# Kernel optimization log

Hardware: AMD Instinct MI355X
Metric: run time of the kernel (lower is better)

The kernel has to match this reference:

```python
import jax, jax.numpy as jnp
import numpy as np
import math

# SH band constants (match torch source)
A0C0 = math.pi * (1.0 / math.sqrt(4.0 * math.pi))
A1C1 = (2.0 * math.pi / math.sqrt(3.0)) * (math.sqrt(3.0) / math.sqrt(4.0 * math.pi))
A2C2 = (2.0 * math.pi / math.sqrt(8.0)) * (3.0 * math.sqrt(5.0) / math.sqrt(12.0 * math.pi))
AMBIENT = 0.8
SIGMA = 1e-4   # BlendParams defaults
GAMMA = 1e-4
BG = (1.0, 1.0, 1.0)
ZNEAR, ZFAR = 1.0, 100.0
EPS = 1e-10

V, F = 100000, 200000
N, H, W, K = 2, 512, 512, 8


def setup_inputs() -> dict:
    key = jax.random.key(0)
    ks = jax.random.split(key, 8)
    verts_normals = jax.random.normal(ks[0], (V, 3), dtype=jnp.float32)
    verts_colors = jax.random.uniform(ks[1], (V, 3), dtype=jnp.float32)
    sh_coeffs = jax.random.normal(ks[2], (1, 9, 3), dtype=jnp.float32) * 0.3
    bary = jax.random.uniform(ks[3], (N, H, W, K, 3), dtype=jnp.float32) + 1e-3
    bary_coords = bary / jnp.sum(bary, axis=-1, keepdims=True)  # convex weights
    zbuf = ZNEAR + (ZFAR - ZNEAR) * jax.random.uniform(ks[4], (N, H, W, K), dtype=jnp.float32)
    dists = jax.random.normal(ks[5], (N, H, W, K), dtype=jnp.float32) * 1e-4  # signed pixel-to-edge dists
    faces = jax.random.randint(ks[6], (F, 3), 0, V, dtype=jnp.int64 if jax.config.jax_enable_x64 else jnp.int32)
    pix_to_face = jax.random.randint(ks[7], (N, H, W, K), -20000, F,
                                     dtype=jnp.int64 if jax.config.jax_enable_x64 else jnp.int32)
    return {"verts_normals": verts_normals, "verts_colors": verts_colors,
            "sh_coeffs": sh_coeffs, "bary_coords": bary_coords,
            "zbuf": zbuf, "dists": dists, "faces": faces, "pix_to_face": pix_to_face}


def _forward(verts_normals, verts_colors, sh_coeffs, bary_coords, zbuf, dists,
             faces, pix_to_face):
    # --- per-vertex SH shading ---
    sh = sh_coeffs.at[..., 0, :].add(AMBIENT)          # (1,9,3), ambient term
    nrm = jnp.maximum(jnp.linalg.norm(verts_normals, axis=-1, keepdims=True), 1e-6)
    n = verts_normals / nrm                            # (V,3)
    nx, ny, nz = n[..., 0], n[..., 1], n[..., 2]
    Y = jnp.stack([
        jnp.full(nx.shape, A0C0, dtype=n.dtype),
        -A1C1 * ny,
        A1C1 * nz,
        -A1C1 * nx,
        A2C2 * nx * ny,
        -A2C2 * ny * nz,
        A2C2 * 0.5 / math.sqrt(3.0) * (3.0 * nz * nz - 1.0),
        -A2C2 * nx * nz,
        A2C2 * 0.5 * (nx * nx - ny * ny),
    ], axis=-1)                                        # (V,9)
    shading = jnp.einsum('vn,nc->vc', Y, sh[0])        # (V,3)
    verts_colors_shaded = verts_colors * shading       # (V,3)

    # --- face gather + barycentric interpolation ---
    face_colors = verts_colors_shaded[faces]           # (F,3,3)
    mask = pix_to_face >= 0                            # (N,H,W,K)
    idx = jnp.where(mask, pix_to_face, 0)
    pix_face_vals = face_colors[idx]                   # (N,H,W,K,3,3)
    colors = jnp.sum(bary_coords[..., None] * pix_face_vals, axis=-2)  # (N,H,W,K,3)
    colors = jnp.where(mask[..., None], colors, 0.0)

    # --- softmax RGB blend ---
    maskf = mask.astype(colors.dtype)
    prob = jax.nn.sigmoid(-dists / SIGMA) * maskf                       # (N,H,W,K)
    alpha = jnp.prod(1.0 - prob, axis=-1)                               # (N,H,W)
    z_inv = (ZFAR - zbuf) / (ZFAR - ZNEAR) * maskf
    z_inv_max = jnp.maximum(jnp.max(z_inv, axis=-1, keepdims=True), EPS)
    weights_num = prob * jnp.exp((z_inv - z_inv_max) / GAMMA)
    delta = jnp.exp((EPS - z_inv_max) / GAMMA)                          # background weight
    denom = jnp.sum(weights_num, axis=-1, keepdims=True) + delta
    weighted_colors = jnp.sum(weights_num[..., None] * colors, axis=-2)  # (N,H,W,3)
    bg = jnp.asarray(BG, dtype=colors.dtype)
    rgb = (weighted_colors + delta * bg) / denom
    return jnp.concatenate([rgb, (1.0 - alpha)[..., None]], axis=-1)    # (N,H,W,4)


def reference(verts_normals, verts_colors, sh_coeffs, bary_coords, zbuf, dists,
              faces, pix_to_face):
    return _forward(verts_normals, verts_colors, sh_coeffs, bary_coords, zbuf,
                    dists, faces, pix_to_face)
```

## Files before the change

### kernel.cpp

```cpp
#include <hip/hip_runtime.h>
#include <math.h>

namespace {

constexpr float kA0C0    = 0.8862269254527580f;
constexpr float kA1C1    = 1.7724538509055159f;
constexpr float kA2C2    = 2.4270324670f;
constexpr float kAmbient = 0.8f;
constexpr float kSigma   = 1e-4f;
constexpr float kGamma   = 1e-4f;
constexpr float kEps     = 1e-10f;
constexpr float kZnear   = 1.0f;
constexpr float kZfar    = 100.0f;
constexpr int   kK       = 8;

__global__ void shade_verts_kernel(const float* __restrict__ vn,
                                   const float* __restrict__ vc,
                                   const float* __restrict__ sh,
                                   float* __restrict__ vs, int V) {
  int v = blockIdx.x * blockDim.x + threadIdx.x;
  if (v >= V) return;
  float nx = vn[3 * v + 0], ny = vn[3 * v + 1], nz = vn[3 * v + 2];
  float nrm = fmaxf(sqrtf(nx * nx + ny * ny + nz * nz), 1e-6f);
  nx /= nrm; ny /= nrm; nz /= nrm;
  float Y[9];
  Y[0] = kA0C0;
  Y[1] = -kA1C1 * ny;
  Y[2] =  kA1C1 * nz;
  Y[3] = -kA1C1 * nx;
  Y[4] =  kA2C2 * nx * ny;
  Y[5] = -kA2C2 * ny * nz;
  Y[6] =  kA2C2 * (0.5f / 1.7320508075688772f) * (3.0f * nz * nz - 1.0f);
  Y[7] = -kA2C2 * nx * nz;
  Y[8] =  kA2C2 * 0.5f * (nx * nx - ny * ny);
#pragma unroll
  for (int c = 0; c < 3; ++c) {
    float s = Y[0] * (sh[0 * 3 + c] + kAmbient);
#pragma unroll
    for (int n = 1; n < 9; ++n) s += Y[n] * sh[n * 3 + c];
    vs[3 * v + c] = vc[3 * v + c] * s;
  }
}

__global__ void face_colors_kernel(const int* __restrict__ faces,
                                   const float* __restrict__ vs,
                                   float* __restrict__ fc, int F) {
  int f = blockIdx.x * blockDim.x + threadIdx.x;
  if (f >= F) return;
  int i0 = faces[3 * f + 0], i1 = faces[3 * f + 1], i2 = faces[3 * f + 2];
#pragma unroll
  for (int c = 0; c < 3; ++c) {
    fc[9 * f + 0 + c] = vs[3 * i0 + c];
    fc[9 * f + 3 + c] = vs[3 * i1 + c];
    fc[9 * f + 6 + c] = vs[3 * i2 + c];
  }
}

template <bool USE_FC>
__global__ void blend_kernel(const float* __restrict__ bary,
                             const float* __restrict__ zbuf,
                             const float* __restrict__ dists,
                             const int* __restrict__ p2f,
                             const float* __restrict__ fc,
                             const int* __restrict__ faces,
                             const float* __restrict__ vs,
                             float* __restrict__ out, int P) {
  int p = blockIdx.x * blockDim.x + threadIdx.x;
  if (p >= P) return;

  int4 fA = reinterpret_cast<const int4*>(p2f)[2 * p];
  int4 fB = reinterpret_cast<const int4*>(p2f)[2 * p + 1];
  int f[8] = {fA.x, fA.y, fA.z, fA.w, fB.x, fB.y, fB.z, fB.w};

  float4 zA = reinterpret_cast<const float4*>(zbuf)[2 * p];
  float4 zB = reinterpret_cast<const float4*>(zbuf)[2 * p + 1];
  float z[8] = {zA.x, zA.y, zA.z, zA.w, zB.x, zB.y, zB.z, zB.w};

  float4 dA = reinterpret_cast<const float4*>(dists)[2 * p];
  float4 dB = reinterpret_cast<const float4*>(dists)[2 * p + 1];
  float d[8] = {dA.x, dA.y, dA.z, dA.w, dB.x, dB.y, dB.z, dB.w};

  float4 b4[6];
#pragma unroll
  for (int i = 0; i < 6; ++i)
    b4[i] = reinterpret_cast<const float4*>(bary)[6 * p + i];
  const float* bw = reinterpret_cast<const float*>(b4);

  float prob[8], zi[8];
  float maxz = kEps;
  float alpha = 1.0f;
#pragma unroll
  for (int k = 0; k < 8; ++k) {
    bool m = f[k] >= 0;
    float pr = m ? (1.0f / (1.0f + expf(d[k] / kSigma))) : 0.0f;
    prob[k] = pr;
    alpha *= (1.0f - pr);
    float zv = m ? ((kZfar - z[k]) / (kZfar - kZnear)) : 0.0f;
    zi[k] = zv;
    maxz = fmaxf(maxz, zv);
  }

  float delta = expf((kEps - maxz) / kGamma);
  float denom = delta;
  float cr = 0.0f, cg = 0.0f, cb = 0.0f;
#pragma unroll
  for (int k = 0; k < 8; ++k) {
    float w = prob[k] * expf((zi[k] - maxz) / kGamma);
    denom += w;
    if (f[k] >= 0 && w != 0.0f) {
      float b0 = bw[3 * k + 0], b1 = bw[3 * k + 1], b2 = bw[3 * k + 2];
      float r, g, b;
      if (USE_FC) {
        const float* fp = fc + 9 * f[k];
        r = b0 * fp[0] + b1 * fp[3] + b2 * fp[6];
        g = b0 * fp[1] + b1 * fp[4] + b2 * fp[7];
        b = b0 * fp[2] + b1 * fp[5] + b2 * fp[8];
      } else {
        int i0 = faces[3 * f[k] + 0], i1 = faces[3 * f[k] + 1], i2 = faces[3 * f[k] + 2];
        r = b0 * vs[3 * i0 + 0] + b1 * vs[3 * i1 + 0] + b2 * vs[3 * i2 + 0];
        g = b0 * vs[3 * i0 + 1] + b1 * vs[3 * i1 + 1] + b2 * vs[3 * i2 + 1];
        b = b0 * vs[3 * i0 + 2] + b1 * vs[3 * i1 + 2] + b2 * vs[3 * i2 + 2];
      }
      cr += w * r; cg += w * g; cb += w * b;
    }
  }

  float4 o;
  o.x = (cr + delta) / denom;
  o.y = (cg + delta) / denom;
  o.z = (cb + delta) / denom;
  o.w = 1.0f - alpha;
  reinterpret_cast<float4*>(out)[p] = o;
}

}

extern "C" void kernel_launch(void* const* d_in, const int* in_sizes, int n_in,
                              void* d_out, int out_size, void* d_ws, size_t ws_size,
                              hipStream_t stream) {
  const float* vn    = (const float*)d_in[0];
  const float* vc    = (const float*)d_in[1];
  const float* sh    = (const float*)d_in[2];
  const float* bary  = (const float*)d_in[3];
  const float* zbuf  = (const float*)d_in[4];
  const float* dists = (const float*)d_in[5];
  const int*   faces = (const int*)d_in[6];
  const int*   p2f   = (const int*)d_in[7];
  float*       out   = (float*)d_out;

  const int V = in_sizes[0] / 3;
  const int F = in_sizes[6] / 3;
  const int P = in_sizes[4] / kK;

  float* vs = (float*)d_ws;
  size_t vsBytes = (size_t)V * 3 * sizeof(float);
  size_t fcOff   = (vsBytes + 255) & ~(size_t)255;
  size_t fcBytes = (size_t)F * 9 * sizeof(float);
  bool useFC = (fcOff + fcBytes) <= ws_size;
  float* fcbuf = (float*)((char*)d_ws + fcOff);

  shade_verts_kernel<<<(V + 255) / 256, 256, 0, stream>>>(vn, vc, sh, vs, V);
  if (useFC) {
    face_colors_kernel<<<(F + 255) / 256, 256, 0, stream>>>(faces, vs, fcbuf, F);
    blend_kernel<true><<<(P + 255) / 256, 256, 0, stream>>>(
        bary, zbuf, dists, p2f, fcbuf, faces, vs, out, P);
  } else {
    blend_kernel<false><<<(P + 255) / 256, 256, 0, stream>>>(
        bary, zbuf, dists, p2f, nullptr, faces, vs, out, P);
  }
}
```

Before: 154.3 us.

## Split blend across 8 lanes per pixel with shuffle reductions and float4 face colors

The blend kernel now assigns one thread per (pixel, k) sample instead of one thread per pixel. Max, product and sum reductions over K run through __shfl_xor, and lane 0 writes the pixel. Face colors are padded to float4 so each vertex color is gathered with one 16-byte load. Divisions become multiplies by reciprocals and __frcp_rn. The per-sample random gathers now come from 8x more threads, which aims to improve latency hiding and coalescing. In exchange it adds shuffle overhead and idle lanes at the store, and removes the fallback for a too-small workspace.

```diff
diff --git a/kernel.cpp b/kernel.cpp
--- a/kernel.cpp
+++ b/kernel.cpp
@@ -7,8 +7,8 @@
 constexpr float kA1C1    = 1.7724538509055159f;
 constexpr float kA2C2    = 2.4270324670f;
 constexpr float kAmbient = 0.8f;
-constexpr float kSigma   = 1e-4f;
-constexpr float kGamma   = 1e-4f;
+constexpr float kInvSigma = 1e4f;
+constexpr float kInvGamma = 1e4f;
 constexpr float kEps     = 1e-10f;
 constexpr float kZnear   = 1.0f;
 constexpr float kZfar    = 100.0f;
@@ -44,93 +44,77 @@
 
 __global__ void face_colors_kernel(const int* __restrict__ faces,
                                    const float* __restrict__ vs,
-                                   float* __restrict__ fc, int F) {
+                                   float4* __restrict__ fc4, int F) {
   int f = blockIdx.x * blockDim.x + threadIdx.x;
   if (f >= F) return;
   int i0 = faces[3 * f + 0], i1 = faces[3 * f + 1], i2 = faces[3 * f + 2];
-#pragma unroll
-  for (int c = 0; c < 3; ++c) {
-    fc[9 * f + 0 + c] = vs[3 * i0 + c];
-    fc[9 * f + 3 + c] = vs[3 * i1 + c];
-    fc[9 * f + 6 + c] = vs[3 * i2 + c];
-  }
+  fc4[3 * f + 0] = make_float4(vs[3 * i0], vs[3 * i0 + 1], vs[3 * i0 + 2], 0.f);
+  fc4[3 * f + 1] = make_float4(vs[3 * i1], vs[3 * i1 + 1], vs[3 * i1 + 2], 0.f);
+  fc4[3 * f + 2] = make_float4(vs[3 * i2], vs[3 * i2 + 1], vs[3 * i2 + 2], 0.f);
 }
 
-template <bool USE_FC>
-__global__ void blend_kernel(const float* __restrict__ bary,
-                             const float* __restrict__ zbuf,
-                             const float* __restrict__ dists,
-                             const int* __restrict__ p2f,
-                             const float* __restrict__ fc,
-                             const int* __restrict__ faces,
-                             const float* __restrict__ vs,
-                             float* __restrict__ out, int P) {
-  int p = blockIdx.x * blockDim.x + threadIdx.x;
-  if (p >= P) return;
+__global__ void __launch_bounds__(256) blend_kernel(
+    const float* __restrict__ bary,
+    const float* __restrict__ zbuf,
+    const float* __restrict__ dists,
+    const int* __restrict__ p2f,
+    const float4* __restrict__ fc4,
+    float4* __restrict__ out, int total) {
+  int t = blockIdx.x * blockDim.x + threadIdx.x;
+  if (t >= total) return;
+  int k = t & 7;
 
-  int4 fA = reinterpret_cast<const int4*>(p2f)[2 * p];
-  int4 fB = reinterpret_cast<const int4*>(p2f)[2 * p + 1];
-  int f[8] = {fA.x, fA.y, fA.z, fA.w, fB.x, fB.y, fB.z, fB.w};
+  int   f = p2f[t];
+  float z = zbuf[t];
+  float d = dists[t];
+  float b0 = bary[3 * t + 0];
+  float b1 = bary[3 * t + 1];
+  float b2 = bary[3 * t + 2];
 
-  float4 zA = reinterpret_cast<const float4*>(zbuf)[2 * p];
-  float4 zB = reinterpret_cast<const float4*>(zbuf)[2 * p + 1];
-  float z[8] = {zA.x, zA.y, zA.z, zA.w, zB.x, zB.y, zB.z, zB.w};
+  bool m = f >= 0;
+  float pr = m ? __frcp_rn(1.0f + expf(d * kInvSigma)) : 0.0f;
+  float zi = m ? (kZfar - z) * (1.0f / (kZfar - kZnear)) : 0.0f;
 
-  float4 dA = reinterpret_cast<const float4*>(dists)[2 * p];
-  float4 dB = reinterpret_cast<const float4*>(dists)[2 * p + 1];
-  float d[8] = {dA.x, dA.y, dA.z, dA.w, dB.x, dB.y, dB.z, dB.w};
+  float maxz = zi;
+#pragma unroll
+  for (int s = 1; s < 8; s <<= 1) maxz = fmaxf(maxz, __shfl_xor(maxz, s));
+  maxz = fmaxf(maxz, kEps);
 
-  float4 b4[6];
+  float one_m = 1.0f - pr;
 #pragma unroll
-  for (int i = 0; i < 6; ++i)
-    b4[i] = reinterpret_cast<const float4*>(bary)[6 * p + i];
-  const float* bw = reinterpret_cast<const float*>(b4);
+  for (int s = 1; s < 8; s <<= 1) one_m *= __shfl_xor(one_m, s);
 
-  float prob[8], zi[8];
-  float maxz = kEps;
-  float alpha = 1.0f;
-#pragma unroll
-  for (int k = 0; k < 8; ++k) {
-    bool m = f[k] >= 0;
-    float pr = m ? (1.0f / (1.0f + expf(d[k] / kSigma))) : 0.0f;
-    prob[k] = pr;
-    alpha *= (1.0f - pr);
-    float zv = m ? ((kZfar - z[k]) / (kZfar - kZnear)) : 0.0f;
-    zi[k] = zv;
-    maxz = fmaxf(maxz, zv);
+  float w = pr * expf((zi - maxz) * kInvGamma);
+  float delta = expf((kEps - maxz) * kInvGamma);
+
+  float cr = 0.0f, cg = 0.0f, cb = 0.0f;
+  if (w != 0.0f) {
+    const float4* fp = fc4 + 3 * f;
+    float4 v0 = fp[0], v1 = fp[1], v2 = fp[2];
+    cr = w * (b0 * v0.x + b1 * v1.x + b2 * v2.x);
+    cg = w * (b0 * v0.y + b1 * v1.y + b2 * v2.y);
+    cb = w * (b0 * v0.z + b1 * v1.z + b2 * v2.z);
   }
 
-  float delta = expf((kEps - maxz) / kGamma);
-  float denom = delta;
-  float cr = 0.0f, cg = 0.0f, cb = 0.0f;
+  float denom = w;
 #pragma unroll
-  for (int k = 0; k < 8; ++k) {
-    float w = prob[k] * expf((zi[k] - maxz) / kGamma);
-    denom += w;
-    if (f[k] >= 0 && w != 0.0f) {
-      float b0 = bw[3 * k + 0], b1 = bw[3 * k + 1], b2 = bw[3 * k + 2];
-      float r, g, b;
-      if (USE_FC) {
-        const float* fp = fc + 9 * f[k];
-        r = b0 * fp[0] + b1 * fp[3] + b2 * fp[6];
-        g = b0 * fp[1] + b1 * fp[4] + b2 * fp[7];
-        b = b0 * fp[2] + b1 * fp[5] + b2 * fp[8];
-      } else {
-        int i0 = faces[3 * f[k] + 0], i1 = faces[3 * f[k] + 1], i2 = faces[3 * f[k] + 2];
-        r = b0 * vs[3 * i0 + 0] + b1 * vs[3 * i1 + 0] + b2 * vs[3 * i2 + 0];
-        g = b0 * vs[3 * i0 + 1] + b1 * vs[3 * i1 + 1] + b2 * vs[3 * i2 + 1];
-        b = b0 * vs[3 * i0 + 2] + b1 * vs[3 * i1 + 2] + b2 * vs[3 * i2 + 2];
-      }
-      cr += w * r; cg += w * g; cb += w * b;
-    }
+  for (int s = 1; s < 8; s <<= 1) {
+    denom += __shfl_xor(denom, s);
+    cr    += __shfl_xor(cr, s);
+    cg    += __shfl_xor(cg, s);
+    cb    += __shfl_xor(cb, s);
   }
 
-  float4 o;
-  o.x = (cr + delta) / denom;
-  o.y = (cg + delta) / denom;
-  o.z = (cb + delta) / denom;
-  o.w = 1.0f - alpha;
-  reinterpret_cast<float4*>(out)[p] = o;
+  if (k == 0) {
+    denom += delta;
+    float inv = __frcp_rn(denom);
+    float4 o;
+    o.x = (cr + delta) * inv;
+    o.y = (cg + delta) * inv;
+    o.z = (cb + delta) * inv;
+    o.w = 1.0f - one_m;
+    out[t >> 3] = o;
+  }
 }
 
 }
@@ -150,22 +134,15 @@
 
   const int V = in_sizes[0] / 3;
   const int F = in_sizes[6] / 3;
-  const int P = in_sizes[4] / kK;
+  const int total = in_sizes[4];
 
   float* vs = (float*)d_ws;
   size_t vsBytes = (size_t)V * 3 * sizeof(float);
   size_t fcOff   = (vsBytes + 255) & ~(size_t)255;
-  size_t fcBytes = (size_t)F * 9 * sizeof(float);
-  bool useFC = (fcOff + fcBytes) <= ws_size;
-  float* fcbuf = (float*)((char*)d_ws + fcOff);
+  float4* fc4    = (float4*)((char*)d_ws + fcOff);
 
   shade_verts_kernel<<<(V + 255) / 256, 256, 0, stream>>>(vn, vc, sh, vs, V);
-  if (useFC) {
-    face_colors_kernel<<<(F + 255) / 256, 256, 0, stream>>>(faces, vs, fcbuf, F);
-    blend_kernel<true><<<(P + 255) / 256, 256, 0, stream>>>(
-        bary, zbuf, dists, p2f, fcbuf, faces, vs, out, P);
-  } else {
-    blend_kernel<false><<<(P + 255) / 256, 256, 0, stream>>>(
-        bary, zbuf, dists, p2f, nullptr, faces, vs, out, P);
-  }
+  face_colors_kernel<<<(F + 255) / 256, 256, 0, stream>>>(faces, vs, fc4, F);
+  blend_kernel<<<(total + 255) / 256, 256, 0, stream>>>(
+      bary, zbuf, dists, p2f, fc4, (float4*)out, total);
 }
```

New measurement: 154.7 us. No clear change (+0.3%).
